# Performance work log

Hardware: AMD Instinct MI355X
Metric: run time of the kernel (lower is better)

The kernel has to match this reference:

```python
import jax, jax.numpy as jnp
from jax import lax
import numpy as np

# constants from module construction: segmentation_loss3D(alpha=1.0, percentile=95)
ALPHA_T = 1.0          # tversky alpha
BETA_T = 2.0 - ALPHA_T # tversky beta
EPS = 1e-5
HD_ALPHA = 2.0         # HausdorffDTLoss default alpha
BIG = 1e9              # stand-in for +inf in the min-plus distance transform


def _dt1d(f, axis):
    """Exact 1D squared Euclidean distance transform along `axis`:
    d[i] = min_j f[j] + (i - j)^2, computed as a min-plus scan over j."""
    n = f.shape[axis]
    fT = jnp.moveaxis(f, axis, 0)                      # (n, ...)
    idx = jnp.arange(n, dtype=f.dtype)
    d0 = jnp.full(fT.shape[1:] + (n,), BIG, f.dtype)   # (..., n)

    def step(d, xs):
        fj, j = xs
        return jnp.minimum(d, fj[..., None] + (idx - j) ** 2), None

    d, _ = lax.scan(step, d0, (fT, idx))
    return jnp.moveaxis(d, -1, axis)


def _edt(mask):
    """Euclidean distance to the nearest False voxel (matches scipy edt),
    over all axes except the two leading (stack, batch) axes."""
    f = jnp.where(mask, jnp.float32(BIG), jnp.float32(0.0))
    for ax in range(2, mask.ndim):
        f = _dt1d(f, ax)
    return jnp.sqrt(f)


def _distance_fields(pred, target_oh):
    # scipy loop runs edt over the full (C, X, Y, Z) array per batch element
    imgs = jnp.stack([pred, target_oh])           # (2, B, C, X, Y, Z)
    fg = imgs > 0.5
    masks = jnp.concatenate([fg, ~fg], axis=0)    # (4, B, C, X, Y, Z)
    dist = _edt(masks)
    field = dist[:2] + dist[2:]                   # fg_dist + bg_dist
    has_fg = jnp.any(fg, axis=(2, 3, 4, 5))       # (2, B) -- torch.no_grad guard
    field = jnp.where(has_fg[:, :, None, None, None, None], field, 0.0)
    field = lax.stop_gradient(field)
    return field[0], field[1]


def setup_inputs() -> dict:
    key = jax.random.key(0)
    k1, k2 = jax.random.split(key)
    B, C, X, Y, Z = 2, 8, 64, 64, 64
    inputs = jax.random.normal(k1, (B, C, X, Y, Z), dtype=jnp.float32)
    targets = jax.random.randint(k2, (B, X, Y, Z), 0, C, dtype=jnp.int32)
    return {"inputs": inputs, "targets": targets}


def reference(inputs, targets):
    C = inputs.shape[1]
    t_oh = jax.nn.one_hot(targets, C, axis=1, dtype=inputs.dtype)  # (B,C,X,Y,Z)

    # --- tversky (dice) loss ---
    probs = jax.nn.softmax(inputs, axis=1)
    red = tuple(range(2, inputs.ndim))
    tps = jnp.sum(probs * t_oh, red)
    fps = jnp.sum(probs * (1.0 - t_oh), red) * ALPHA_T
    fns = jnp.sum((1.0 - probs) * t_oh, red) * BETA_T
    score = 2.0 * tps / (2.0 * tps + fps + fns + EPS)   # (B, C)
    dice = 1.0 - jnp.mean(score, axis=0)[1:].mean()

    # --- cross entropy (mean over all voxels) ---
    logp = jax.nn.log_softmax(inputs, axis=1)
    ce = -jnp.mean(jnp.take_along_axis(logp, targets[:, None].astype(jnp.int32), axis=1))

    # --- Hausdorff distance-transform loss ---
    pred_dt, target_dt = _distance_fields(inputs, t_oh)
    pred_error = (inputs - t_oh) ** 2
    distance = pred_dt ** HD_ALPHA + target_dt ** HD_ALPHA
    hd = jnp.mean(pred_error * distance)

    return dice + ce + hd
```

## Files before the change

### kernel.cpp

```cpp
#include <hip/hip_runtime.h>

#define NVOX (64 * 64 * 64)
#define FMU (16 * NVOX)
#define FM (16 * NVOX)


__device__ __forceinline__ float unpack_val(unsigned short p) {
    int v = p & 0x7fff;
    return (v == 32767) ? 1e9f : (float)v;
}


__global__ __launch_bounds__(256) void k_zy2(const float* __restrict__ in,
                                             const int* __restrict__ tg,
                                             unsigned short* __restrict__ f) {
    __shared__ float tile[64 * 65];
    int blk = blockIdx.x;
    int src = blk >> 10;
    int s = blk & 1023;
    int b = s >> 9, c = (s >> 6) & 7, x = s & 63;
    int w = threadIdx.x >> 6;
    int z = threadIdx.x & 63;

    const float* pin = in + (b * 8 + c) * NVOX + x * 4096;
    const int* ptg = tg + b * NVOX + x * 4096;

    float dA[16], dB[16];
    bool mb[16];
#pragma unroll
    for (int k = 0; k < 16; ++k) {
        int y = k * 4 + w;
        bool member;
        if (src == 0) member = pin[y * 64 + z] > 0.5f;
        else          member = ptg[y * 64 + z] == c;
        mb[k] = member;
        unsigned long long mkA = __ballot(!member);
        unsigned long long mkB = ~mkA;
        unsigned long long sfA = mkA << (63 - z), sbA = mkA >> z;
        int dfA = sfA ? __builtin_clzll(sfA) : 64;
        int dbA = sbA ? __builtin_ctzll(sbA) : 64;
        int da = dfA < dbA ? dfA : dbA;
        unsigned long long sfB = mkB << (63 - z), sbB = mkB >> z;
        int dfB = sfB ? __builtin_clzll(sfB) : 64;
        int dbB = sbB ? __builtin_ctzll(sbB) : 64;
        int db = dfB < dbB ? dfB : dbB;
        float a2 = (da > 63) ? 1e9f : (float)(da * da);
        float b2 = (db > 63) ? 1e9f : (float)(db * db);
        tile[y * 65 + z] = a2;
        dA[k] = a2;
        dB[k] = b2;
    }
    __syncthreads();

    float rA[16];
#pragma unroll
    for (int k = 0; k < 16; ++k) {
        int y = k * 4 + w;
        float d = dA[k];
        int q = 1;
        for (int dd = 1; dd <= 63 && (float)q < d; ++dd) {
            int jl = y - dd, jr = y + dd;
            float cl = (jl >= 0) ? tile[jl * 65 + z] : 1e9f;
            float cr = (jr < 64) ? tile[jr * 65 + z] : 1e9f;
            d = fminf(d, fminf(cl, cr) + (float)q);
            q += 2 * dd + 1;
        }
        rA[k] = fminf(d, 1e9f);
    }
    __syncthreads();
#pragma unroll
    for (int k = 0; k < 16; ++k) tile[(k * 4 + w) * 65 + z] = dB[k];
    __syncthreads();

    unsigned short* out = f + (size_t)src * FMU + (b * 8 + c) * NVOX + x * 4096;
#pragma unroll
    for (int k = 0; k < 16; ++k) {
        int y = k * 4 + w;
        float d = dB[k];
        int q = 1;
        for (int dd = 1; dd <= 63 && (float)q < d; ++dd) {
            int jl = y - dd, jr = y + dd;
            float cl = (jl >= 0) ? tile[jl * 65 + z] : 1e9f;
            float cr = (jr < 64) ? tile[jr * 65 + z] : 1e9f;
            d = fminf(d, fminf(cl, cr) + (float)q);
            q += 2 * dd + 1;
        }
        float tot = rA[k] + fminf(d, 1e9f);
        int vi = (int)fminf(tot, 32767.f);
        out[y * 64 + z] = (unsigned short)((mb[k] ? 0x8000 : 0) | vi);
    }
}

__global__ __launch_bounds__(256) void k_xdt(unsigned short* __restrict__ f) {
    __shared__ float tile[64 * 65];
    int blk = blockIdx.x;
    int src = blk >> 10;
    int s = blk & 1023;
    int b = s >> 9, c = (s >> 6) & 7, y = s & 63;
    int w = threadIdx.x >> 6;
    int z = threadIdx.x & 63;

    unsigned short* base = f + (size_t)src * FMU + (b * 8 + c) * NVOX + y * 64;

    unsigned short pk[16];
    float dA0[16], dB0[16];
#pragma unroll
    for (int k = 0; k < 16; ++k) {
        int x = k * 4 + w;
        unsigned short p = base[x * 4096 + z];
        pk[k] = p;
        float fv = unpack_val(p);
        bool member = (p & 0x8000) != 0;
        float a = member ? fv : 0.f;
        float bb = member ? 0.f : fv;
        tile[x * 65 + z] = a;
        dA0[k] = a;
        dB0[k] = bb;
    }
    __syncthreads();

    float rA[16];
#pragma unroll
    for (int k = 0; k < 16; ++k) {
        int x = k * 4 + w;
        float d = dA0[k];
        int q = 1;
        for (int dd = 1; dd <= 63 && (float)q < d; ++dd) {
            int jl = x - dd, jr = x + dd;
            float cl = (jl >= 0) ? tile[jl * 65 + z] : 1e9f;
            float cr = (jr < 64) ? tile[jr * 65 + z] : 1e9f;
            d = fminf(d, fminf(cl, cr) + (float)q);
            q += 2 * dd + 1;
        }
        rA[k] = fminf(d, 1e9f);
    }
    __syncthreads();
#pragma unroll
    for (int k = 0; k < 16; ++k) tile[(k * 4 + w) * 65 + z] = dB0[k];
    __syncthreads();

#pragma unroll
    for (int k = 0; k < 16; ++k) {
        int x = k * 4 + w;
        float d = dB0[k];
        int q = 1;
        for (int dd = 1; dd <= 63 && (float)q < d; ++dd) {
            int jl = x - dd, jr = x + dd;
            float cl = (jl >= 0) ? tile[jl * 65 + z] : 1e9f;
            float cr = (jr < 64) ? tile[jr * 65 + z] : 1e9f;
            d = fminf(d, fminf(cl, cr) + (float)q);
            q += 2 * dd + 1;
        }
        float tot = rA[k] + fminf(d, 1e9f);
        int vi = (int)fminf(tot, 32767.f);
        base[x * 4096 + z] = (unsigned short)((pk[k] & 0x8000) | vi);
    }
}

__global__ __launch_bounds__(256) void k_chds(const float* __restrict__ in,
                                              const int* __restrict__ tg,
                                              const unsigned short* __restrict__ f,
                                              float* __restrict__ statP,
                                              double* __restrict__ predS,
                                              double* __restrict__ tgtS) {
    __shared__ float part[4][27];
    __shared__ int af;
    if (threadIdx.x == 0) af = 0;
    __syncthreads();

    int blk = blockIdx.x;
    int v = blk * 256 + threadIdx.x;
    int b = v >> 18;
    int r = v & (NVOX - 1);
    int t = tg[v];
    int lane = threadIdx.x & 63;
    int wid = threadIdx.x >> 6;

    float xs[8];
#pragma unroll
    for (int c = 0; c < 8; ++c) xs[c] = in[(b * 8 + c) * NVOX + r];
    float mx = xs[0];
#pragma unroll
    for (int c = 1; c < 8; ++c) mx = fmaxf(mx, xs[c]);
    float se = 0.f;
#pragma unroll
    for (int c = 0; c < 8; ++c) se += expf(xs[c] - mx);
    float inv = 1.f / se;
    float lse = mx + logf(se);
    float xt = xs[0];
#pragma unroll
    for (int c = 1; c < 8; ++c) xt = (t == c) ? xs[c] : xt;

    bool anyP = false;
    float red[25];
#pragma unroll
    for (int c = 0; c < 8; ++c) {
        float p = expf(xs[c] - mx) * inv;
        red[c] = p;
        red[8 + c] = (t == c) ? p : 0.f;
        red[16 + c] = (t == c) ? 1.f : 0.f;
        anyP = anyP || (xs[c] > 0.5f);
    }
    red[24] = lse - xt;

#pragma unroll
    for (int k = 0; k < 25; ++k) {
        float s = red[k];
        s += __shfl_down(s, 32);
        s += __shfl_down(s, 16);
        s += __shfl_down(s, 8);
        s += __shfl_down(s, 4);
        s += __shfl_down(s, 2);
        s += __shfl_down(s, 1);
        red[k] = s;
    }
    bool wav = __any(anyP);
    if (lane == 0) {
#pragma unroll
        for (int k = 0; k < 25; ++k) part[wid][k] = red[k];
        if (wav) atomicOr(&af, 1);
    }

    float e2[8];
#pragma unroll
    for (int c = 0; c < 8; ++c) {
        float e = xs[c] - ((t == c) ? 1.f : 0.f);
        e2[c] = e * e;
    }
    float accP = 0.f, accT = 0.f;
#pragma unroll
    for (int src = 0; src < 2; ++src) {
        float fmA[8], fmB[8];
#pragma unroll
        for (int c = 0; c < 8; ++c) {
            unsigned short p = f[(size_t)src * FMU + (b * 8 + c) * NVOX + r];
            float fv = unpack_val(p);
            bool member = (p & 0x8000) != 0;
            fmA[c] = member ? fv : 0.f;
            fmB[c] = member ? 0.f : fv;
        }
        float am = 0.f;
#pragma unroll
        for (int i = 0; i < 8; ++i) {
            float da = 1e9f, db = 1e9f;
#pragma unroll
            for (int j = 0; j < 8; ++j) {
                float q = (float)((i - j) * (i - j));
                da = fminf(da, fmA[j] + q);
                db = fminf(db, fmB[j] + q);
            }
            am += e2[i] * (da + db);
        }
        if (src) accT += am; else accP += am;
    }
#pragma unroll
    for (int off = 32; off >= 1; off >>= 1) {
        accP += __shfl_down(accP, off);
        accT += __shfl_down(accT, off);
    }
    if (lane == 0) { part[wid][25] = accP; part[wid][26] = accT; }
    __syncthreads();

    int j = blk & 1023;
    if (threadIdx.x < 25)
        statP[(b * 26 + threadIdx.x) * 1024 + j] =
            part[0][threadIdx.x] + part[1][threadIdx.x] +
            part[2][threadIdx.x] + part[3][threadIdx.x];
    if (threadIdx.x == 25)
        statP[(b * 26 + 25) * 1024 + j] = af ? 1.f : 0.f;
    if (threadIdx.x == 26)
        predS[blk] = (double)part[0][25] + (double)part[1][25] +
                     (double)part[2][25] + (double)part[3][25];
    if (threadIdx.x == 27)
        tgtS[blk] = (double)part[0][26] + (double)part[1][26] +
                    (double)part[2][26] + (double)part[3][26];
}

__global__ __launch_bounds__(256) void k_final3(const float* __restrict__ statP,
                                                const double* __restrict__ predS,
                                                const double* __restrict__ tgtS,
                                                float* __restrict__ out) {
    __shared__ float rs[52];
    __shared__ double rd[4];
    int tid = threadIdx.x;
    int w = tid >> 6;
    int lane = tid & 63;

    for (int row = w; row < 52; row += 4) {
        const float* p = statP + row * 1024;
        float s = 0.f;
#pragma unroll
        for (int k = 0; k < 16; ++k) s += p[k * 64 + lane];
        s += __shfl_down(s, 32);
        s += __shfl_down(s, 16);
        s += __shfl_down(s, 8);
        s += __shfl_down(s, 4);
        s += __shfl_down(s, 2);
        s += __shfl_down(s, 1);
        if (lane == 0) rs[row] = s;
    }
    {
        const double* p = (w < 2) ? (predS + w * 1024) : (tgtS + (w - 2) * 1024);
        double s = 0.0;
#pragma unroll
        for (int k = 0; k < 16; ++k) s += p[k * 64 + lane];
        s += __shfl_down(s, 32);
        s += __shfl_down(s, 16);
        s += __shfl_down(s, 8);
        s += __shfl_down(s, 4);
        s += __shfl_down(s, 2);
        s += __shfl_down(s, 1);
        if (lane == 0) rd[w] = s;
    }
    __syncthreads();

    if (tid == 0) {
        bool fP0 = rs[0 * 26 + 25] > 0.f;
        bool fP1 = rs[1 * 26 + 25] > 0.f;
        double h = (fP0 ? rd[0] : 0.0) + (fP1 ? rd[1] : 0.0) + rd[2] + rd[3];
        float dsum = 0.f;
        for (int c = 1; c < 8; ++c) {
            float sc = 0.f;
            for (int b = 0; b < 2; ++b) {
                float S1 = rs[b * 26 + c];
                float S2 = rs[b * 26 + 8 + c];
                float Nc = rs[b * 26 + 16 + c];
                sc += 2.f * S2 / (2.f * S2 + (S1 - S2) + (Nc - S2) + 1e-5f);
            }
            dsum += sc * 0.5f;
        }
        float dice = 1.f - dsum / 7.f;
        float ce = (rs[0 * 26 + 24] + rs[1 * 26 + 24]) / 524288.f;
        out[0] = dice + ce + (float)(h / 4194304.0);
    }
}

__global__ __launch_bounds__(256, 4) void k_stats(const float* __restrict__ in,
                                                  const int* __restrict__ tg,
                                                  float* __restrict__ accF,
                                                  int* __restrict__ flags) {
    int r = blockIdx.x * 256 + threadIdx.x;
    int lane = threadIdx.x & 63;
    int wid = threadIdx.x >> 6;
    __shared__ float part[4][25];
    __shared__ int af;

    for (int b = 0; b < 2; ++b) {
        int t = tg[b * NVOX + r];
        float xs[8];
#pragma unroll
        for (int c = 0; c < 8; ++c) xs[c] = in[(b * 8 + c) * NVOX + r];
        float mx = xs[0];
#pragma unroll
        for (int c = 1; c < 8; ++c) mx = fmaxf(mx, xs[c]);
        float ex[8];
        float se = 0.f;
#pragma unroll
        for (int c = 0; c < 8; ++c) { ex[c] = expf(xs[c] - mx); se += ex[c]; }
        float inv = 1.f / se;
        float lse = mx + logf(se);
        float xt = xs[0];
#pragma unroll
        for (int c = 1; c < 8; ++c) xt = (t == c) ? xs[c] : xt;
        bool anyP = false;
        float red[25];
#pragma unroll
        for (int c = 0; c < 8; ++c) {
            float p = ex[c] * inv;
            red[c] = p;
            red[8 + c] = (t == c) ? p : 0.f;
            red[16 + c] = (t == c) ? 1.f : 0.f;
            anyP = anyP || (xs[c] > 0.5f);
        }
        red[24] = lse - xt;
#pragma unroll
        for (int k = 0; k < 25; ++k) {
            float s = red[k];
            s += __shfl_down(s, 32);
            s += __shfl_down(s, 16);
            s += __shfl_down(s, 8);
            s += __shfl_down(s, 4);
            s += __shfl_down(s, 2);
            s += __shfl_down(s, 1);
            red[k] = s;
        }
        if (threadIdx.x == 0) af = 0;
        __syncthreads();
        bool wav = __any(anyP);
        if (lane == 0) {
#pragma unroll
            for (int k = 0; k < 25; ++k) part[wid][k] = red[k];
            if (wav) atomicOr(&af, 1);
        }
        __syncthreads();
        if (threadIdx.x < 25) {
            float s = part[0][threadIdx.x] + part[1][threadIdx.x] +
                      part[2][threadIdx.x] + part[3][threadIdx.x];
            atomicAdd(&accF[b * 25 + threadIdx.x], s);
        }
        if (threadIdx.x == 0 && af) atomicOr(&flags[b], 1);
        __syncthreads();
    }
}

template <int M0>
__global__ __launch_bounds__(64) void k_mask_zy(const float* __restrict__ in,
                                                const int* __restrict__ tg,
                                                float* __restrict__ f) {
    __shared__ float tile[64 * 65];
    int blk = blockIdx.x;
    int m = M0 + (blk >> 10);
    int s = blk & 1023;
    int b = s >> 9, c = (s >> 6) & 7, x = s & 63;
    int tid = threadIdx.x;

    if ((m & 1) == 0) {
        const float* src = in + (b * 8 + c) * NVOX + x * 4096;
#pragma unroll 8
        for (int k = 0; k < 64; ++k) {
            bool fg = src[k * 64 + tid] > 0.5f;
            bool hot = (m < 2) ? fg : !fg;
            tile[k * 65 + tid] = hot ? 1e9f : 0.f;
        }
    } else {
        const int* src = tg + b * NVOX + x * 4096;
#pragma unroll 8
        for (int k = 0; k < 64; ++k) {
            bool fg = (src[k * 64 + tid] == c);
            bool hot = (m < 2) ? fg : !fg;
            tile[k * 65 + tid] = hot ? 1e9f : 0.f;
        }
    }
    __syncthreads();
    {
        float* row = &tile[tid * 65];
        float g = 1000.f;
#pragma unroll 8
        for (int z = 0; z < 64; ++z) {
            float v = row[z];
            g = (v == 0.f) ? 0.f : g + 1.f;
            row[z] = g;
        }
        g = 1000.f;
#pragma unroll 8
        for (int z = 63; z >= 0; --z) {
            float gf = row[z];
            g = (gf == 0.f) ? 0.f : g + 1.f;
            float d = fminf(gf, g);
            row[z] = (d > 63.f) ? 1e9f : d * d;
        }
    }
    __syncthreads();
    float* out = f + (size_t)(blk >> 10) * FM + (b * 8 + c) * NVOX + x * 4096;
    for (int i = 0; i < 64; ++i) {
        float d0 = tile[i * 65 + tid];
        float d = d0;
        int Ri = (int)sqrtf(d0) + 1;
        Ri = (Ri > 63) ? 63 : Ri;
        for (int dd = 1; dd <= Ri; ++dd) {
            float q = (float)(dd * dd);
            int jl = i - dd, jr = i + dd;
            float cl = (jl >= 0) ? tile[jl * 65 + tid] : 1e9f;
            float cr = (jr < 64) ? tile[jr * 65 + tid] : 1e9f;
            d = fminf(d, fminf(cl, cr) + q);
        }
        out[i * 64 + tid] = fminf(d, 1e9f);
    }
}

template <int M0>
__global__ __launch_bounds__(128, 4) void k_dtx(float* __restrict__ f) {
    __shared__ float wl[128 * 65];
    int blk = blockIdx.x;
    int mi = blk >> 9;
    int s = blk & 511;
    int plane = s >> 5;
    int y0 = (s & 31) * 2;
    int tid = threadIdx.x;
    float* fb = f + (size_t)mi * FM + plane * NVOX + y0 * 64;

#pragma unroll 8
    for (int j = 0; j < 64; ++j) wl[tid * 65 + j] = fb[j * 4096 + tid];

    float* row = &wl[tid * 65];
    for (int i = 0; i < 64; ++i) {
        float d0 = row[i];
        float d = d0;
        int Ri = (int)sqrtf(d0) + 1;
        Ri = (Ri > 63) ? 63 : Ri;
        for (int dd = 1; dd <= Ri; ++dd) {
            float q = (float)(dd * dd);
            int jl = i - dd, jr = i + dd;
            float cl = (jl >= 0) ? row[jl] : 1e9f;
            float cr = (jr < 64) ? row[jr] : 1e9f;
            d = fminf(d, fminf(cl, cr) + q);
        }
        fb[i * 4096 + tid] = fminf(d, 1e9f);
    }
}

template <int M0, int NM>
__global__ __launch_bounds__(256, 4) void k_cdt_hd(const float* __restrict__ in,
                                                   const int* __restrict__ tg,
                                                   const float* __restrict__ f,
                                                   const int* __restrict__ flags,
                                                   double* __restrict__ hd) {
    int v = blockIdx.x * 256 + threadIdx.x;
    int b = v >> 18;
    int r = v & (NVOX - 1);
    int t = tg[v];

    float e2[8];
#pragma unroll
    for (int c = 0; c < 8; ++c) {
        float e = in[(b * 8 + c) * NVOX + r] - ((t == c) ? 1.f : 0.f);
        e2[c] = e * e;
    }
    float acc = 0.f;
#pragma unroll
    for (int mi = 0; mi < NM; ++mi) {
        int m = M0 + mi;
        float fl = (m & 1) ? 1.f : (flags[b] ? 1.f : 0.f);
        float fm[8];
#pragma unroll
        for (int c = 0; c < 8; ++c)
            fm[c] = f[(size_t)mi * FM + (b * 8 + c) * NVOX + r];
        float am = 0.f;
#pragma unroll
        for (int i = 0; i < 8; ++i) {
            float d = 1e9f;
#pragma unroll
            for (int j = 0; j < 8; ++j)
                d = fminf(d, fm[j] + (float)((i - j) * (i - j)));
            am += e2[i] * d;
        }
        acc += fl * am;
    }
    float ssum = acc;
    ssum += __shfl_down(ssum, 32);
    ssum += __shfl_down(ssum, 16);
    ssum += __shfl_down(ssum, 8);
    ssum += __shfl_down(ssum, 4);
    ssum += __shfl_down(ssum, 2);
    ssum += __shfl_down(ssum, 1);
    __shared__ float part[4];
    int lane = threadIdx.x & 63;
    int wid = threadIdx.x >> 6;
    if (lane == 0) part[wid] = ssum;
    __syncthreads();
    if (threadIdx.x == 0)
        atomicAdd(hd, (double)(part[0] + part[1] + part[2] + part[3]));
}

__global__ void k_final(const float* __restrict__ accF,
                        const double* __restrict__ hd,
                        float* __restrict__ out) {
    float dsum = 0.f;
    for (int c = 1; c < 8; ++c) {
        float sc = 0.f;
        for (int b = 0; b < 2; ++b) {
            float S1 = accF[b * 25 + c];
            float S2 = accF[b * 25 + 8 + c];
            float Nc = accF[b * 25 + 16 + c];
            sc += 2.f * S2 / (2.f * S2 + (S1 - S2) + (Nc - S2) + 1e-5f);
        }
        dsum += sc * 0.5f;
    }
    float dice = 1.f - dsum / 7.f;
    float ce = (accF[24] + accF[25 + 24]) / 524288.f;
    float hdv = (float)(hd[0] / 4194304.0);
    out[0] = dice + ce + hdv;
}

template <int M0, int NM>
static void run_chunk(const float* in, const int* tg, float* f,
                      const int* flags, double* hd, hipStream_t stream) {
    k_mask_zy<M0><<<NM * 1024, 64, 0, stream>>>(in, tg, f);
    k_dtx<M0><<<NM * 512, 128, 0, stream>>>(f);
    k_cdt_hd<M0, NM><<<2048, 256, 0, stream>>>(in, tg, f, flags, hd);
}

extern "C" void kernel_launch(void* const* d_in, const int* in_sizes, int n_in,
                              void* d_out, int out_size, void* d_ws, size_t ws_size,
                              hipStream_t stream) {
    const float* in = (const float*)d_in[0];
    const int* tg = (const int*)d_in[1];
    float* out = (float*)d_out;

    size_t offF = (size_t)2 * FMU * 2;
    size_t need_fast = offF + 16384 + 16384 + 52 * 1024 * 4;

    if (ws_size >= need_fast) {
        unsigned short* fu = (unsigned short*)d_ws;
        double* predS = (double*)((char*)d_ws + offF);
        double* tgtS = (double*)((char*)d_ws + offF + 16384);
        float* statP = (float*)((char*)d_ws + offF + 32768);
        k_zy2<<<2048, 256, 0, stream>>>(in, tg, fu);
        k_xdt<<<2048, 256, 0, stream>>>(fu);
        k_chds<<<2048, 256, 0, stream>>>(in, tg, fu, statP, predS, tgtS);
        k_final3<<<1, 256, 0, stream>>>(statP, predS, tgtS, out);
    } else {
        float* f = (float*)d_ws;
        size_t acc_off = ((ws_size - 256) / 256) * 256;
        char* accB = (char*)d_ws + acc_off;
        double* hd = (double*)accB;
        float* accF = (float*)(accB + 8);
        int* flags = (int*)(accB + 208);
        hipMemsetAsync(accB, 0, 256, stream);
        k_stats<<<1024, 256, 0, stream>>>(in, tg, accF, flags);
        int nm_cap = (int)(acc_off / ((size_t)FM * 4));
        if (nm_cap >= 2) {
            run_chunk<0, 2>(in, tg, f, flags, hd, stream);
            run_chunk<2, 2>(in, tg, f, flags, hd, stream);
        } else if (nm_cap >= 1) {
            run_chunk<0, 1>(in, tg, f, flags, hd, stream);
            run_chunk<1, 1>(in, tg, f, flags, hd, stream);
            run_chunk<2, 1>(in, tg, f, flags, hd, stream);
            run_chunk<3, 1>(in, tg, f, flags, hd, stream);
        }
        k_final<<<1, 1, 0, stream>>>(accF, hd, out);
    }
}
```

Baseline: 144.3 us.

## Transpose DT scan mapping so lanes walk rows, stage outputs through LDS

```diff
diff --git a/kernel.cpp b/kernel.cpp
--- a/kernel.cpp
+++ b/kernel.cpp
@@ -15,51 +15,47 @@
                                              const int* __restrict__ tg,
                                              unsigned short* __restrict__ f) {
     __shared__ float tile[64 * 65];
+    unsigned short* tile16 = (unsigned short*)tile;
     int blk = blockIdx.x;
     int src = blk >> 10;
     int s = blk & 1023;
     int b = s >> 9, c = (s >> 6) & 7, x = s & 63;
     int w = threadIdx.x >> 6;
-    int z = threadIdx.x & 63;
+    int lane = threadIdx.x & 63;
 
     const float* pin = in + (b * 8 + c) * NVOX + x * 4096;
     const int* ptg = tg + b * NVOX + x * 4096;
 
-    float dA[16], dB[16];
-    bool mb[16];
+    float dB[16];
 #pragma unroll
     for (int k = 0; k < 16; ++k) {
         int y = k * 4 + w;
         bool member;
-        if (src == 0) member = pin[y * 64 + z] > 0.5f;
-        else          member = ptg[y * 64 + z] == c;
-        mb[k] = member;
+        if (src == 0) member = pin[y * 64 + lane] > 0.5f;
+        else          member = ptg[y * 64 + lane] == c;
         unsigned long long mkA = __ballot(!member);
         unsigned long long mkB = ~mkA;
-        unsigned long long sfA = mkA << (63 - z), sbA = mkA >> z;
+        unsigned long long sfA = mkA << (63 - lane), sbA = mkA >> lane;
         int dfA = sfA ? __builtin_clzll(sfA) : 64;
         int dbA = sbA ? __builtin_ctzll(sbA) : 64;
         int da = dfA < dbA ? dfA : dbA;
-        unsigned long long sfB = mkB << (63 - z), sbB = mkB >> z;
+        unsigned long long sfB = mkB << (63 - lane), sbB = mkB >> lane;
         int dfB = sfB ? __builtin_clzll(sfB) : 64;
         int dbB = sbB ? __builtin_ctzll(sbB) : 64;
         int db = dfB < dbB ? dfB : dbB;
-        float a2 = (da > 63) ? 1e9f : (float)(da * da);
-        float b2 = (db > 63) ? 1e9f : (float)(db * db);
-        tile[y * 65 + z] = a2;
-        dA[k] = a2;
-        dB[k] = b2;
+        tile[y * 65 + lane] = (da > 63) ? 1e9f : (float)(da * da);
+        dB[k] = (db > 63) ? 1e9f : (float)(db * db);
     }
     __syncthreads();
 
     float rA[16];
 #pragma unroll
     for (int k = 0; k < 16; ++k) {
-        int y = k * 4 + w;
-        float d = dA[k];
+        int z = k * 4 + w;
+        float d = tile[lane * 65 + z];
         int q = 1;
         for (int dd = 1; dd <= 63 && (float)q < d; ++dd) {
-            int jl = y - dd, jr = y + dd;
+            int jl = lane - dd, jr = lane + dd;
             float cl = (jl >= 0) ? tile[jl * 65 + z] : 1e9f;
             float cr = (jr < 64) ? tile[jr * 65 + z] : 1e9f;
             d = fminf(d, fminf(cl, cr) + (float)q);
@@ -68,65 +64,78 @@
         rA[k] = fminf(d, 1e9f);
     }
     __syncthreads();
-#pragma unroll
-    for (int k = 0; k < 16; ++k) tile[(k * 4 + w) * 65 + z] = dB[k];
-    __syncthreads();
-
-    unsigned short* out = f + (size_t)src * FMU + (b * 8 + c) * NVOX + x * 4096;
-#pragma unroll
-    for (int k = 0; k < 16; ++k) {
-        int y = k * 4 + w;
-        float d = dB[k];
+
+#pragma unroll
+    for (int k = 0; k < 16; ++k) tile[(k * 4 + w) * 65 + lane] = dB[k];
+    __syncthreads();
+
+    float rB[16];
+#pragma unroll
+    for (int k = 0; k < 16; ++k) {
+        int z = k * 4 + w;
+        float d = tile[lane * 65 + z];
         int q = 1;
         for (int dd = 1; dd <= 63 && (float)q < d; ++dd) {
-            int jl = y - dd, jr = y + dd;
+            int jl = lane - dd, jr = lane + dd;
             float cl = (jl >= 0) ? tile[jl * 65 + z] : 1e9f;
             float cr = (jr < 64) ? tile[jr * 65 + z] : 1e9f;
             d = fminf(d, fminf(cl, cr) + (float)q);
             q += 2 * dd + 1;
         }
-        float tot = rA[k] + fminf(d, 1e9f);
+        rB[k] = fminf(d, 1e9f);
+    }
+    __syncthreads();
+
+#pragma unroll
+    for (int k = 0; k < 16; ++k) {
+        int z = k * 4 + w;
+        float tot = rA[k] + rB[k];
         int vi = (int)fminf(tot, 32767.f);
-        out[y * 64 + z] = (unsigned short)((mb[k] ? 0x8000 : 0) | vi);
+        tile16[lane * 65 + z] =
+            (unsigned short)(((rB[k] == 0.f) ? 0x8000 : 0) | vi);
+    }
+    __syncthreads();
+
+    unsigned short* out = f + (size_t)src * FMU + (b * 8 + c) * NVOX + x * 4096;
+#pragma unroll
+    for (int k = 0; k < 16; ++k) {
+        int y = k * 4 + w;
+        out[y * 64 + lane] = tile16[y * 65 + lane];
     }
 }
 
 __global__ __launch_bounds__(256) void k_xdt(unsigned short* __restrict__ f) {
     __shared__ float tile[64 * 65];
+    unsigned short* tile16 = (unsigned short*)tile;
     int blk = blockIdx.x;
     int src = blk >> 10;
     int s = blk & 1023;
     int b = s >> 9, c = (s >> 6) & 7, y = s & 63;
     int w = threadIdx.x >> 6;
-    int z = threadIdx.x & 63;
+    int lane = threadIdx.x & 63;
 
     unsigned short* base = f + (size_t)src * FMU + (b * 8 + c) * NVOX + y * 64;
 
-    unsigned short pk[16];
-    float dA0[16], dB0[16];
+    float dB0[16];
 #pragma unroll
     for (int k = 0; k < 16; ++k) {
         int x = k * 4 + w;
-        unsigned short p = base[x * 4096 + z];
-        pk[k] = p;
+        unsigned short p = base[x * 4096 + lane];
         float fv = unpack_val(p);
         bool member = (p & 0x8000) != 0;
-        float a = member ? fv : 0.f;
-        float bb = member ? 0.f : fv;
-        tile[x * 65 + z] = a;
-        dA0[k] = a;
-        dB0[k] = bb;
+        tile[x * 65 + lane] = member ? fv : 0.f;
+        dB0[k] = member ? 0.f : fv;
     }
     __syncthreads();
 
     float rA[16];
 #pragma unroll
     for (int k = 0; k < 16; ++k) {
-        int x = k * 4 + w;
-        float d = dA0[k];
+        int z = k * 4 + w;
+        float d = tile[lane * 65 + z];
         int q = 1;
         for (int dd = 1; dd <= 63 && (float)q < d; ++dd) {
-            int jl = x - dd, jr = x + dd;
+            int jl = lane - dd, jr = lane + dd;
             float cl = (jl >= 0) ? tile[jl * 65 + z] : 1e9f;
             float cr = (jr < 64) ? tile[jr * 65 + z] : 1e9f;
             d = fminf(d, fminf(cl, cr) + (float)q);
@@ -135,25 +144,42 @@
         rA[k] = fminf(d, 1e9f);
     }
     __syncthreads();
-#pragma unroll
-    for (int k = 0; k < 16; ++k) tile[(k * 4 + w) * 65 + z] = dB0[k];
-    __syncthreads();
-
-#pragma unroll
-    for (int k = 0; k < 16; ++k) {
-        int x = k * 4 + w;
-        float d = dB0[k];
+
+#pragma unroll
+    for (int k = 0; k < 16; ++k) tile[(k * 4 + w) * 65 + lane] = dB0[k];
+    __syncthreads();
+
+    float rB[16];
+#pragma unroll
+    for (int k = 0; k < 16; ++k) {
+        int z = k * 4 + w;
+        float d = tile[lane * 65 + z];
         int q = 1;
         for (int dd = 1; dd <= 63 && (float)q < d; ++dd) {
-            int jl = x - dd, jr = x + dd;
+            int jl = lane - dd, jr = lane + dd;
             float cl = (jl >= 0) ? tile[jl * 65 + z] : 1e9f;
             float cr = (jr < 64) ? tile[jr * 65 + z] : 1e9f;
             d = fminf(d, fminf(cl, cr) + (float)q);
             q += 2 * dd + 1;
         }
-        float tot = rA[k] + fminf(d, 1e9f);
+        rB[k] = fminf(d, 1e9f);
+    }
+    __syncthreads();
+
+#pragma unroll
+    for (int k = 0; k < 16; ++k) {
+        int z = k * 4 + w;
+        float tot = rA[k] + rB[k];
         int vi = (int)fminf(tot, 32767.f);
-        base[x * 4096 + z] = (unsigned short)((pk[k] & 0x8000) | vi);
+        tile16[lane * 65 + z] =
+            (unsigned short)(((rB[k] == 0.f) ? 0x8000 : 0) | vi);
+    }
+    __syncthreads();
+
+#pragma unroll
+    for (int k = 0; k < 16; ++k) {
+        int x = k * 4 + w;
+        base[x * 4096 + lane] = tile16[x * 65 + lane];
     }
 }
 
@@ -176,7 +202,7 @@
     int lane = threadIdx.x & 63;
     int wid = threadIdx.x >> 6;
 
-    float xs[8];
+    float xs[8], ex[8];
 #pragma unroll
     for (int c = 0; c < 8; ++c) xs[c] = in[(b * 8 + c) * NVOX + r];
     float mx = xs[0];
@@ -184,7 +210,7 @@
     for (int c = 1; c < 8; ++c) mx = fmaxf(mx, xs[c]);
     float se = 0.f;
 #pragma unroll
-    for (int c = 0; c < 8; ++c) se += expf(xs[c] - mx);
+    for (int c = 0; c < 8; ++c) { ex[c] = expf(xs[c] - mx); se += ex[c]; }
     float inv = 1.f / se;
     float lse = mx + logf(se);
     float xt = xs[0];
@@ -192,19 +218,20 @@
     for (int c = 1; c < 8; ++c) xt = (t == c) ? xs[c] : xt;
 
     bool anyP = false;
-    float red[25];
+    float red[17];
+    float cnt[8];
 #pragma unroll
     for (int c = 0; c < 8; ++c) {
-        float p = expf(xs[c] - mx) * inv;
+        float p = ex[c] * inv;
         red[c] = p;
         red[8 + c] = (t == c) ? p : 0.f;
-        red[16 + c] = (t == c) ? 1.f : 0.f;
+        cnt[c] = (float)__popcll(__ballot(t == c));
         anyP = anyP || (xs[c] > 0.5f);
     }
-    red[24] = lse - xt;
-
-#pragma unroll
-    for (int k = 0; k < 25; ++k) {
+    red[16] = lse - xt;
+
+#pragma unroll
+    for (int k = 0; k < 17; ++k) {
         float s = red[k];
         s += __shfl_down(s, 32);
         s += __shfl_down(s, 16);
@@ -217,7 +244,12 @@
     bool wav = __any(anyP);
     if (lane == 0) {
 #pragma unroll
-        for (int k = 0; k < 25; ++k) part[wid][k] = red[k];
+        for (int k = 0; k < 8; ++k) part[wid][k] = red[k];
+#pragma unroll
+        for (int k = 0; k < 8; ++k) part[wid][8 + k] = red[8 + k];
+#pragma unroll
+        for (int k = 0; k < 8; ++k) part[wid][16 + k] = cnt[k];
+        part[wid][24] = red[16];
         if (wav) atomicOr(&af, 1);
     }
 
```

After: 139.8 us. 1.03x faster.
